# Kernel tuning notes

Hardware: AMD Instinct MI355X
Metric: run time of the kernel (lower is better)

Reference implementation:

```python
import jax, jax.numpy as jnp
import numpy as np


def setup_inputs() -> dict:
    key = jax.random.key(0)
    k1, k2, k3 = jax.random.split(key, 3)
    B, T, I, H = 32, 2048, 512, 512
    x = jax.random.normal(k1, (B, T, I), dtype=jnp.float32)
    W_x = jax.random.normal(k2, (3, I, H), dtype=jnp.float32) / np.sqrt(I)
    W_h = jax.random.normal(k3, (3, H, H), dtype=jnp.float32) / np.sqrt(H)
    bias = jnp.zeros((3, H), dtype=jnp.float32)
    return {"x": x, "W_x": W_x, "W_h": W_h, "bias": bias}


def reference(x, W_x, W_h, bias):
    # x: [B, T, I]; W_x: [3, I, H]; W_h: [3, H, H]; bias: [3, H]
    B, T, I = x.shape
    H = W_h.shape[-1]
    # Precompute input-side contributions for all gates/timesteps (batched GEMM):
    # gx: [T, 3, B, H] = x @ W_x[g] + bias[g]
    gx = jnp.einsum('bti,gih->tgbh', x, W_x) + bias[:, None, :]

    W_hz, W_hr, W_hh = W_h[0], W_h[1], W_h[2]

    def step(h_prev, gx_t):
        # gx_t: [3, B, H]
        z = jax.nn.sigmoid(gx_t[0] + h_prev @ W_hz)          # update gate
        r = jax.nn.sigmoid(gx_t[1] + h_prev @ W_hr)          # reset gate
        h_tilde = jnp.tanh(gx_t[2] + (r * h_prev) @ W_hh)    # candidate
        h_t = (1.0 - z) * h_prev + z * h_tilde
        return h_t, h_t

    h0 = jnp.zeros((B, H), dtype=x.dtype)
    h_last, outs = jax.lax.scan(step, h0, gx)  # outs: [T, B, H]
    output = jnp.transpose(outs, (1, 0, 2))    # [B, T, H]
    return output, h_last
```

## Files before the change

kernel.cpp:

```cpp
#include <hip/hip_runtime.h>
#include <stdint.h>
#include <stddef.h>


#define AGENT __HIP_MEMORY_SCOPE_AGENT

typedef _Float16 h2v __attribute__((ext_vector_type(2)));
typedef _Float16 half8 __attribute__((ext_vector_type(8)));
typedef float f32x4 __attribute__((ext_vector_type(4)));

__device__ __forceinline__ uint32_t pk2u(float a, float b) {
  h2v r; r[0] = (_Float16)a; r[1] = (_Float16)b;
  return __builtin_bit_cast(uint32_t, r);
}
__device__ __forceinline__ h2v bc2(uint32_t u) { return __builtin_bit_cast(h2v, u); }
__device__ __forceinline__ float dot2f(h2v a, h2v b, float c) {
#if __has_builtin(__builtin_amdgcn_fdot2)
  return __builtin_amdgcn_fdot2(a, b, c, false);
#else
  return fmaf((float)a[1], (float)b[1], fmaf((float)a[0], (float)b[0], c));
#endif
}
__device__ __forceinline__ float sigmoidf_(float x) { return 1.0f / (1.0f + __expf(-x)); }
__device__ __forceinline__ float tanhf_(float x) { return 1.0f - 2.0f / (1.0f + __expf(2.0f * x)); }
__device__ __forceinline__ uint64_t ald64(const uint64_t* p) {
  return __hip_atomic_load(p, __ATOMIC_RELAXED, AGENT);
}
__device__ __forceinline__ void ast64(uint64_t* p, uint64_t v) {
  __hip_atomic_store(p, v, __ATOMIC_RELAXED, AGENT);
}

__global__ __launch_bounds__(256) void gemm_gx(const float* __restrict__ x,
                                               const float* __restrict__ Wx,
                                               const float* __restrict__ bias,
                                               _Float16* gzr,
                                               _Float16* gh,
                                               int nTN) {
  __shared__ alignas(16) _Float16 Alds[128 * 68];
  __shared__ alignas(16) _Float16 Blds[128 * 68];
  const int tid = threadIdx.x;
  const int bid = blockIdx.x;
  const int tm = bid / nTN, tn = bid % nTN;
  const int m0 = tm << 7, n0 = tn << 7;
  const int lane = tid & 63;
  const int wv = tid >> 6, wm = wv >> 1, wn = wv & 1;
  const int l15 = lane & 15, lhi = lane >> 4;
  f32x4 acc[4][4] = {};

  for (int k0 = 0; k0 < 512; k0 += 64) {
#pragma unroll
    for (int r = 0; r < 8; ++r) {
      int m = r * 16 + (tid >> 4);
      int k = (tid & 15) * 4;
      float4 v = *(const float4*)&x[(size_t)(m0 + m) * 512 + k0 + k];
      union { _Float16 h[4]; uint2 u; } cv;
      cv.h[0] = (_Float16)v.x; cv.h[1] = (_Float16)v.y;
      cv.h[2] = (_Float16)v.z; cv.h[3] = (_Float16)v.w;
      *(uint2*)&Alds[m * 68 + k] = cv.u;
    }
#pragma unroll
    for (int u = 0; u < 8; ++u) {
      int n = tid & 127;
      int k = (tid >> 7) * 32 + u * 4;
      int ng = n0 + n;
      const float* wp = Wx + ((size_t)(ng >> 9) << 18) + (size_t)(k0 + k) * 512 + (ng & 511);
      union { _Float16 h[4]; uint2 u2; } cv;
      cv.h[0] = (_Float16)wp[0];    cv.h[1] = (_Float16)wp[512];
      cv.h[2] = (_Float16)wp[1024]; cv.h[3] = (_Float16)wp[1536];
      *(uint2*)&Blds[n * 68 + k] = cv.u2;
    }
    __syncthreads();
#pragma unroll
    for (int kk = 0; kk < 2; ++kk) {
      int q = kk * 4 + lhi;
      half8 af[4], bf[4];
#pragma unroll
      for (int fm = 0; fm < 4; ++fm) {
        const _Float16* pa = &Alds[(wm * 64 + fm * 16 + l15) * 68 + q * 8];
        union { uint2 u[2]; half8 h; } cv;
        cv.u[0] = *(const uint2*)pa; cv.u[1] = *(const uint2*)(pa + 4);
        af[fm] = cv.h;
      }
#pragma unroll
      for (int fn = 0; fn < 4; ++fn) {
        const _Float16* pb = &Blds[(wn * 64 + fn * 16 + l15) * 68 + q * 8];
        union { uint2 u[2]; half8 h; } cv;
        cv.u[0] = *(const uint2*)pb; cv.u[1] = *(const uint2*)(pb + 4);
        bf[fn] = cv.h;
      }
#pragma unroll
      for (int fm = 0; fm < 4; ++fm)
#pragma unroll
        for (int fn = 0; fn < 4; ++fn)
          acc[fm][fn] = __builtin_amdgcn_mfma_f32_16x16x32_f16(af[fm], bf[fn], acc[fm][fn], 0, 0, 0);
    }
    __syncthreads();
  }
#pragma unroll
  for (int fn = 0; fn < 4; ++fn) {
    int col = n0 + wn * 64 + fn * 16 + l15;
    float bv = bias[col];
#pragma unroll
    for (int fm = 0; fm < 4; ++fm) {
#pragma unroll
      for (int q2 = 0; q2 < 4; ++q2) {
        int row = m0 + wm * 64 + fm * 16 + lhi * 4 + q2;
        _Float16 val = (_Float16)(acc[fm][fn][q2] + bv);
        if (n0 < 1024) gzr[(size_t)row * 1024 + col] = val;
        else           gh[(size_t)row * 512 + (col - 1024)] = val;
      }
    }
  }
}

template <bool GH>
__global__ __launch_bounds__(512) void gru_scan(
    const float* __restrict__ x,
    const float* __restrict__ Wx,
    const float* __restrict__ Wh,
    const float* __restrict__ bias,
    const _Float16* gzr,
    const _Float16* gh,
    float* out,
    uint64_t* __restrict__ Pbuf,
    uint64_t* __restrict__ zbuf) {
  __shared__ alignas(16) float zrp[2][8][64];
  __shared__ alignas(16) _Float16 wzr[2 * 64 * 516];
  __shared__ alignas(16) _Float16 h16[512];
  __shared__ alignas(16) _Float16 rh16[64];
  __shared__ alignas(16) _Float16 x16s[64];

  const int T = threadIdx.x;
  const int bid = blockIdx.x;
  const int xcd = bid & 7, ii = bid >> 3;
  const int batch = xcd * 4 + (ii >> 3);
  const int slice = ii & 7;
  const int wv = T >> 6;
  const int ln = T & 63;
  const int n = T;

  {
    const int cc = T & 63, kb = T >> 6;
#pragma unroll 4
    for (int g = 0; g < 2; ++g) {
      const float* W = Wh + (size_t)g * 262144 + slice * 64 + cc;
      for (int i = 0; i < 64; ++i) {
        int k = kb + 8 * i;
        wzr[(g * 64 + cc) * 516 + k] = (_Float16)W[(size_t)k * 512];
      }
    }
  }
  uint32_t wh2[32], wx2[GH ? 1 : 32];
  {
    const float* Whh = Wh + 524288;
#pragma unroll
    for (int j = 0; j < 32; ++j) {
      int kk = slice * 64 + 2 * j;
      wh2[j] = pk2u(Whh[(size_t)kk * 512 + n], Whh[(size_t)(kk + 1) * 512 + n]);
    }
    if (!GH) {
      const float* Wxh = Wx + 524288;
#pragma unroll
      for (int j = 0; j < 32; ++j) {
        int kk = slice * 64 + 2 * j;
        wx2[j] = pk2u(Wxh[(size_t)kk * 512 + n], Wxh[(size_t)(kk + 1) * 512 + n]);
      }
    }
  }
  const float bh = bias[1024 + n];

  float hreg = 0.0f;
  h16[T] = (_Float16)0.0f;

  const size_t rowbase = (size_t)batch * 2048;
  float gz_p = 0.f, gr_p = 0.f, gz_cur = 0.f, gr_cur = 0.f, x_p = 0.f;
  float gh_p = 0.f, gh_cur = 0.f;
  if (T < 64)       gz_p = (float)gzr[rowbase * 1024 + slice * 64 + T];
  else if (T < 128) gr_p = (float)gzr[rowbase * 1024 + 512 + slice * 64 + (T - 64)];
  if (GH) gh_p = (float)gh[rowbase * 512 + n];
  else if (T < 64) x_p = x[rowbase * 512 + slice * 64 + T];

  uint64_t* Pmine = Pbuf + ((size_t)batch * 8 + slice) * 512 + n;
  const uint64_t* Pread = Pbuf + ((size_t)batch * 8) * 512 + n;
  uint64_t* zmine = zbuf + (size_t)batch * 512 + slice * 64 + ln;
  const uint64_t* zread = zbuf + (size_t)batch * 512 + n;

  for (int t = 0; t < 2048; ++t) {
    if (t > 0) {
      const size_t po = ((t - 1) & 1) ? 131072 : 0;
      const size_t zo = ((t - 1) & 1) ? 16384 : 0;
      const uint32_t want = (uint32_t)t;
      uint64_t v[8];
#pragma unroll
      for (int g = 0; g < 8; ++g) v[g] = ald64(Pread + po + (size_t)g * 512);
      uint64_t zv = ald64(zread + zo);
      for (;;) {
        bool ok = true;
        if ((uint32_t)(zv >> 32) != want) { zv = ald64(zread + zo); ok = false; }
#pragma unroll
        for (int g = 0; g < 8; ++g)
          if ((uint32_t)(v[g] >> 32) != want) { v[g] = ald64(Pread + po + (size_t)g * 512); ok = false; }
        if (ok) break;
        __builtin_amdgcn_s_sleep(1);
      }
      float hsum = 0.f;
#pragma unroll
      for (int g = 0; g < 8; ++g) hsum += __uint_as_float((uint32_t)v[g]);
      float zf = __uint_as_float((uint32_t)zv);
      float htil = tanhf_(GH ? (gh_cur + hsum) : (bh + hsum));
      float hn = fmaf(zf, htil - hreg, hreg);
      if (slice == 0) out[(rowbase + (t - 1)) * 512 + n] = hn;
      hreg = hn;
      h16[T] = (_Float16)hn;
    }
    gz_cur = gz_p; gr_cur = gr_p;
    if (GH) gh_cur = gh_p;
    else if (T < 64) x16s[T] = (_Float16)x_p;
    __syncthreads();
    if (t < 2047) {
      size_t r1 = rowbase + t + 1;
      if (T < 64)       gz_p = (float)gzr[r1 * 1024 + slice * 64 + T];
      else if (T < 128) gr_p = (float)gzr[r1 * 1024 + 512 + slice * 64 + (T - 64)];
      if (GH) gh_p = (float)gh[r1 * 512 + n];
      else if (T < 64) x_p = x[r1 * 512 + slice * 64 + T];
    }

    float za = 0.f, ra = 0.f;
    {
      const _Float16* wzp = &wzr[(0 * 64 + ln) * 516 + 64 * wv];
      const _Float16* wrp = &wzr[(1 * 64 + ln) * 516 + 64 * wv];
      const _Float16* hp = &h16[64 * wv];
#pragma unroll
      for (int j = 0; j < 16; ++j) {
        uint2 wzu = *(const uint2*)(wzp + 4 * j);
        uint2 wru = *(const uint2*)(wrp + 4 * j);
        uint2 hu = *(const uint2*)(hp + 4 * j);
        za = dot2f(bc2(hu.x), bc2(wzu.x), za);
        za = dot2f(bc2(hu.y), bc2(wzu.y), za);
        ra = dot2f(bc2(hu.x), bc2(wru.x), ra);
        ra = dot2f(bc2(hu.y), bc2(wru.y), ra);
      }
    }
    zrp[0][wv][ln] = za;
    zrp[1][wv][ln] = ra;
    __syncthreads();
    const size_t po = (t & 1) ? 131072 : 0;
    const size_t zo = (t & 1) ? 16384 : 0;
    const uint64_t tagw = ((uint64_t)(uint32_t)(t + 1)) << 32;
    if (T < 128) {
      const int g = T >> 6, c = T & 63;
      float sum = 0.f;
#pragma unroll
      for (int s2 = 0; s2 < 8; ++s2) sum += zrp[g][s2][c];
      if (g == 0) {
        float z = sigmoidf_(sum + gz_cur);
        ast64(zmine + zo, tagw | (uint32_t)__float_as_uint(z));
      } else {
        float r = sigmoidf_(sum + gr_cur);
        rh16[c] = (_Float16)(r * (float)h16[slice * 64 + c]);
      }
    }
    __syncthreads();

    float pa = 0.f;
#pragma unroll
    for (int j = 0; j < 16; ++j) {
      uint2 ru = *(const uint2*)&rh16[4 * j];
      pa = dot2f(bc2(ru.x), bc2(wh2[2 * j]), pa);
      pa = dot2f(bc2(ru.y), bc2(wh2[2 * j + 1]), pa);
    }
    if (!GH) {
#pragma unroll
      for (int j = 0; j < 16; ++j) {
        uint2 xu = *(const uint2*)&x16s[4 * j];
        pa = dot2f(bc2(xu.x), bc2(wx2[2 * j]), pa);
        pa = dot2f(bc2(xu.y), bc2(wx2[2 * j + 1]), pa);
      }
    }
    ast64(Pmine + po, tagw | (uint32_t)__float_as_uint(pa));
    if (!GH) __syncthreads();
  }

  {
    const uint32_t want = 2048u;
    uint64_t v[8];
#pragma unroll
    for (int g = 0; g < 8; ++g) v[g] = ald64(Pread + 131072 + (size_t)g * 512);
    uint64_t zv = ald64(zread + 16384);
    for (;;) {
      bool ok = true;
      if ((uint32_t)(zv >> 32) != want) { zv = ald64(zread + 16384); ok = false; }
#pragma unroll
      for (int g = 0; g < 8; ++g)
        if ((uint32_t)(v[g] >> 32) != want) { v[g] = ald64(Pread + 131072 + (size_t)g * 512); ok = false; }
      if (ok) break;
      __builtin_amdgcn_s_sleep(1);
    }
    float hsum = 0.f;
#pragma unroll
    for (int g = 0; g < 8; ++g) hsum += __uint_as_float((uint32_t)v[g]);
    float zf = __uint_as_float((uint32_t)zv);
    float htil = tanhf_(GH ? (gh_cur + hsum) : (bh + hsum));
    float hn = fmaf(zf, htil - hreg, hreg);
    if (slice == 0) {
      out[(rowbase + 2047) * 512 + n] = hn;
      out[(size_t)32 * 2048 * 512 + (size_t)batch * 512 + n] = hn;
    }
  }
}

extern "C" void kernel_launch(void* const* d_in, const int* in_sizes, int n_in,
                              void* d_out, int out_size, void* d_ws, size_t ws_size,
                              hipStream_t stream) {
  (void)in_sizes; (void)n_in; (void)out_size;
  const float* x    = (const float*)d_in[0];
  const float* Wx   = (const float*)d_in[1];
  const float* Wh   = (const float*)d_in[2];
  const float* bias = (const float*)d_in[3];
  float* out = (float*)d_out;
  char* ws = (char*)d_ws;

  uint64_t* Pbuf = (uint64_t*)ws;
  uint64_t* zbuf = (uint64_t*)(ws + 2097152);
  _Float16* gh   = (_Float16*)(ws + 2621440);

  hipMemsetAsync(ws, 0, 2621440, stream);
  const bool gh_mode = ws_size >= (size_t)2621440 + 67108864ull;
  if (gh_mode) {
    gemm_gx<<<512 * 12, 256, 0, stream>>>(x, Wx, bias, (_Float16*)d_out, gh, 12);
    gru_scan<true><<<256, 512, 0, stream>>>(x, Wx, Wh, bias, (const _Float16*)d_out,
                                            gh, out, Pbuf, zbuf);
  } else {
    gemm_gx<<<512 * 8, 256, 0, stream>>>(x, Wx, bias, (_Float16*)d_out, gh, 8);
    gru_scan<false><<<256, 512, 0, stream>>>(x, Wx, Wh, bias, (const _Float16*)d_out,
                                             gh, out, Pbuf, zbuf);
  }
}
```

Measured before the change: 7.110 ms.

## Split hidden dim over 16 blocks, interleave two batches per block

The persistent GRU scan kernel is restructured so each of 256 blocks owns a 32-column slice of the hidden state for two batches (16 slices per batch) instead of a 64-column slice for one batch. The two batches are processed in an interleaved way, so the cross-block wait for one batch's partial sums overlaps with compute for the other. The candidate partial sums are exchanged as fp16 values tagged with a 16-bit step number packed into 32-bit words, which halves exchange traffic. In exchange each step now reduces 16 partials instead of 8, adds more synchronisation points and lowers the precision of the exchanged partials.

```diff
diff --git a/kernel.cpp b/kernel.cpp
--- a/kernel.cpp
+++ b/kernel.cpp
@@ -23,11 +23,21 @@
 }
 __device__ __forceinline__ float sigmoidf_(float x) { return 1.0f / (1.0f + __expf(-x)); }
 __device__ __forceinline__ float tanhf_(float x) { return 1.0f - 2.0f / (1.0f + __expf(2.0f * x)); }
+
+__device__ __forceinline__ uint32_t ald32(const uint32_t* p) {
+  return __hip_atomic_load(p, __ATOMIC_RELAXED, AGENT);
+}
+__device__ __forceinline__ void ast32(uint32_t* p, uint32_t v) {
+  __hip_atomic_store(p, v, __ATOMIC_RELAXED, AGENT);
+}
 __device__ __forceinline__ uint64_t ald64(const uint64_t* p) {
   return __hip_atomic_load(p, __ATOMIC_RELAXED, AGENT);
 }
 __device__ __forceinline__ void ast64(uint64_t* p, uint64_t v) {
   __hip_atomic_store(p, v, __ATOMIC_RELAXED, AGENT);
+}
+__device__ __forceinline__ float f16b2f(uint32_t w) {
+  return (float)__builtin_bit_cast(_Float16, (unsigned short)(w & 0xffffu));
 }
 
 __global__ __launch_bounds__(256) void gemm_gx(const float* __restrict__ x,
@@ -113,19 +123,293 @@
   }
 }
 
-template <bool GH>
-__global__ __launch_bounds__(512) void gru_scan(
-    const float* __restrict__ x,
-    const float* __restrict__ Wx,
+__device__ __forceinline__ bool tagsok(const uint32_t pv[16], uint64_t zv, uint32_t want) {
+  bool ok = ((uint32_t)(zv >> 32) == want);
+#pragma unroll
+  for (int q = 0; q < 16; ++q) ok &= ((pv[q] >> 16) == want);
+  return ok;
+}
+
+__global__ __launch_bounds__(512) void gru_scan2(
+    const _Float16* gzr,
+    const _Float16* ghg,
     const float* __restrict__ Wh,
-    const float* __restrict__ bias,
-    const _Float16* gzr,
-    const _Float16* gh,
     float* out,
-    uint64_t* __restrict__ Pbuf,
+    uint32_t* __restrict__ Pbuf,
     uint64_t* __restrict__ zbuf) {
+  __shared__ alignas(16) _Float16 wzK[2 * 64 * 32 * 8];
+  __shared__ alignas(16) _Float16 hA[512], hB[512];
+  __shared__ alignas(16) _Float16 rhA[32], rhB[32];
+  __shared__ alignas(16) float zrp[2][16][32];
+
+  const int T = threadIdx.x;
+  const int bid = blockIdx.x;
+  const int s = bid >> 4;
+  const int p = bid & 15;
+  const int c0 = s * 32;
+  const int bA = p, bB = p + 16;
+  const int j = T & 31, sub = T >> 5;
+
+  for (int g = 0; g < 2; ++g) {
+    const float* W = Wh + (size_t)g * 262144;
+    for (int kc = sub; kc < 64; kc += 16) {
+#pragma unroll
+      for (int e = 0; e < 8; ++e) {
+        int k = kc * 8 + e;
+        wzK[((g * 64 + kc) * 32 + j) * 8 + e] = (_Float16)W[(size_t)k * 512 + c0 + j];
+      }
+    }
+  }
+  uint32_t wh2[16];
+  {
+    const float* Whh = Wh + 524288;
+#pragma unroll
+    for (int i = 0; i < 16; ++i) {
+      int kk = c0 + 2 * i;
+      wh2[i] = pk2u(Whh[(size_t)kk * 512 + T], Whh[(size_t)(kk + 1) * 512 + T]);
+    }
+  }
+  hA[T] = (_Float16)0.0f;
+  hB[T] = (_Float16)0.0f;
+  float hregA = 0.f, hregB = 0.f;
+
+  const size_t rbA = (size_t)bA * 2048, rbB = (size_t)bB * 2048;
+  float gzA_p = 0.f, grA_p = 0.f, gzB_p = 0.f, grB_p = 0.f;
+  float gzA_c = 0.f, grA_c = 0.f, gzB_c = 0.f, grB_c = 0.f;
+  float ghA_p, ghB_p, ghA_c = 0.f, ghB_c = 0.f;
+  if (T < 32) {
+    gzA_p = (float)gzr[rbA * 1024 + c0 + T];
+    gzB_p = (float)gzr[rbB * 1024 + c0 + T];
+  } else if (T < 64) {
+    grA_p = (float)gzr[rbA * 1024 + 512 + c0 + (T - 32)];
+    grB_p = (float)gzr[rbB * 1024 + 512 + c0 + (T - 32)];
+  }
+  ghA_p = (float)ghg[rbA * 512 + T];
+  ghB_p = (float)ghg[rbB * 512 + T];
+
+  uint32_t* PmA = Pbuf + ((size_t)bA * 512 + T) * 16 + s;
+  uint32_t* PmB = Pbuf + ((size_t)bB * 512 + T) * 16 + s;
+  const uint32_t* PrA = Pbuf + ((size_t)bA * 512 + T) * 16;
+  const uint32_t* PrB = Pbuf + ((size_t)bB * 512 + T) * 16;
+  uint64_t* zmA = zbuf + (size_t)bA * 512 + c0 + (T & 31);
+  uint64_t* zmB = zbuf + (size_t)bB * 512 + c0 + (T & 31);
+  const uint64_t* zrdA = zbuf + (size_t)bA * 512 + T;
+  const uint64_t* zrdB = zbuf + (size_t)bB * 512 + T;
+
+  uint32_t pvA[16], pvB[16];
+  uint64_t zvA = 0, zvB = 0;
+#pragma unroll
+  for (int q = 0; q < 16; ++q) { pvA[q] = 0; pvB[q] = 0; }
+
+  for (int t = 0; t < 2048; ++t) {
+    const size_t poC = ((t - 1) & 1) ? 262144 : 0;
+    const size_t zoC = ((t - 1) & 1) ? 16384 : 0;
+    const size_t poN = (t & 1) ? 262144 : 0;
+    const size_t zoN = (t & 1) ? 16384 : 0;
+    const uint32_t want = (uint32_t)t;
+    const uint32_t tagN = (uint32_t)(t + 1);
+
+    if (t > 0) {
+      while (!tagsok(pvA, zvA, want)) {
+        __builtin_amdgcn_s_sleep(1);
+        zvA = ald64(zrdA + zoC);
+#pragma unroll
+        for (int q = 0; q < 16; ++q)
+          if ((pvA[q] >> 16) != want) pvA[q] = ald32(PrA + poC + q);
+      }
+      float hsum = 0.f;
+#pragma unroll
+      for (int q = 0; q < 16; ++q) hsum += f16b2f(pvA[q]);
+      float zf = __uint_as_float((uint32_t)zvA);
+      float htil = tanhf_(ghA_c + hsum);
+      float hn = fmaf(zf, htil - hregA, hregA);
+      if (sub == s) out[(rbA + (t - 1)) * 512 + T] = hn;
+      hregA = hn;
+      hA[T] = (_Float16)hn;
+    }
+    gzA_c = gzA_p; grA_c = grA_p; ghA_c = ghA_p;
+    __syncthreads();
+    if (t < 2047) {
+      size_t r1 = rbA + t + 1;
+      if (T < 32)      gzA_p = (float)gzr[r1 * 1024 + c0 + T];
+      else if (T < 64) grA_p = (float)gzr[r1 * 1024 + 512 + c0 + (T - 32)];
+      ghA_p = (float)ghg[r1 * 512 + T];
+    }
+    {
+      float za = 0.f, ra = 0.f;
+#pragma unroll
+      for (int cc = 0; cc < 4; ++cc) {
+        int kc = sub * 4 + cc;
+        uint4 hu = *(const uint4*)&hA[kc * 8];
+        uint4 wz = *(const uint4*)&wzK[(kc * 32 + j) * 8];
+        uint4 wr = *(const uint4*)&wzK[((64 + kc) * 32 + j) * 8];
+        za = dot2f(bc2(hu.x), bc2(wz.x), za); za = dot2f(bc2(hu.y), bc2(wz.y), za);
+        za = dot2f(bc2(hu.z), bc2(wz.z), za); za = dot2f(bc2(hu.w), bc2(wz.w), za);
+        ra = dot2f(bc2(hu.x), bc2(wr.x), ra); ra = dot2f(bc2(hu.y), bc2(wr.y), ra);
+        ra = dot2f(bc2(hu.z), bc2(wr.z), ra); ra = dot2f(bc2(hu.w), bc2(wr.w), ra);
+      }
+      zrp[0][sub][j] = za;
+      zrp[1][sub][j] = ra;
+    }
+    if (t > 0) {
+      zvB = ald64(zrdB + zoC);
+#pragma unroll
+      for (int q = 0; q < 16; ++q) pvB[q] = ald32(PrB + poC + q);
+    }
+    __syncthreads();
+    if (T < 64) {
+      const int g = T >> 5, jj = T & 31;
+      float sum = 0.f;
+#pragma unroll
+      for (int q = 0; q < 16; ++q) sum += zrp[g][q][jj];
+      if (g == 0) {
+        float z = sigmoidf_(sum + gzA_c);
+        ast64(zmA + zoN, ((uint64_t)tagN << 32) | (uint32_t)__float_as_uint(z));
+      } else {
+        float r = sigmoidf_(sum + grA_c);
+        rhA[jj] = (_Float16)(r * (float)hA[c0 + jj]);
+      }
+    }
+    __syncthreads();
+    {
+      float pa = 0.f;
+#pragma unroll
+      for (int i = 0; i < 8; ++i) {
+        uint2 ru = *(const uint2*)&rhA[4 * i];
+        pa = dot2f(bc2(ru.x), bc2(wh2[2 * i]), pa);
+        pa = dot2f(bc2(ru.y), bc2(wh2[2 * i + 1]), pa);
+      }
+      unsigned short pb = __builtin_bit_cast(unsigned short, (_Float16)pa);
+      ast32(PmA + poN, (tagN << 16) | (uint32_t)pb);
+    }
+
+    if (t > 0) {
+      while (!tagsok(pvB, zvB, want)) {
+        __builtin_amdgcn_s_sleep(1);
+        zvB = ald64(zrdB + zoC);
+#pragma unroll
+        for (int q = 0; q < 16; ++q)
+          if ((pvB[q] >> 16) != want) pvB[q] = ald32(PrB + poC + q);
+      }
+      float hsum = 0.f;
+#pragma unroll
+      for (int q = 0; q < 16; ++q) hsum += f16b2f(pvB[q]);
+      float zf = __uint_as_float((uint32_t)zvB);
+      float htil = tanhf_(ghB_c + hsum);
+      float hn = fmaf(zf, htil - hregB, hregB);
+      if (sub == s) out[(rbB + (t - 1)) * 512 + T] = hn;
+      hregB = hn;
+      hB[T] = (_Float16)hn;
+    }
+    gzB_c = gzB_p; grB_c = grB_p; ghB_c = ghB_p;
+    __syncthreads();
+    if (t < 2047) {
+      size_t r1 = rbB + t + 1;
+      if (T < 32)      gzB_p = (float)gzr[r1 * 1024 + c0 + T];
+      else if (T < 64) grB_p = (float)gzr[r1 * 1024 + 512 + c0 + (T - 32)];
+      ghB_p = (float)ghg[r1 * 512 + T];
+    }
+    {
+      float za = 0.f, ra = 0.f;
+#pragma unroll
+      for (int cc = 0; cc < 4; ++cc) {
+        int kc = sub * 4 + cc;
+        uint4 hu = *(const uint4*)&hB[kc * 8];
+        uint4 wz = *(const uint4*)&wzK[(kc * 32 + j) * 8];
+        uint4 wr = *(const uint4*)&wzK[((64 + kc) * 32 + j) * 8];
+        za = dot2f(bc2(hu.x), bc2(wz.x), za); za = dot2f(bc2(hu.y), bc2(wz.y), za);
+        za = dot2f(bc2(hu.z), bc2(wz.z), za); za = dot2f(bc2(hu.w), bc2(wz.w), za);
+        ra = dot2f(bc2(hu.x), bc2(wr.x), ra); ra = dot2f(bc2(hu.y), bc2(wr.y), ra);
+        ra = dot2f(bc2(hu.z), bc2(wr.z), ra); ra = dot2f(bc2(hu.w), bc2(wr.w), ra);
+      }
+      zrp[0][sub][j] = za;
+      zrp[1][sub][j] = ra;
+    }
+    {
+      zvA = ald64(zrdA + zoN);
+#pragma unroll
+      for (int q = 0; q < 16; ++q) pvA[q] = ald32(PrA + poN + q);
+    }
+    __syncthreads();
+    if (T < 64) {
+      const int g = T >> 5, jj = T & 31;
+      float sum = 0.f;
+#pragma unroll
+      for (int q = 0; q < 16; ++q) sum += zrp[g][q][jj];
+      if (g == 0) {
+        float z = sigmoidf_(sum + gzB_c);
+        ast64(zmB + zoN, ((uint64_t)tagN << 32) | (uint32_t)__float_as_uint(z));
+      } else {
+        float r = sigmoidf_(sum + grB_c);
+        rhB[jj] = (_Float16)(r * (float)hB[c0 + jj]);
+      }
+    }
+    __syncthreads();
+    {
+      float pa = 0.f;
+#pragma unroll
+      for (int i = 0; i < 8; ++i) {
+        uint2 ru = *(const uint2*)&rhB[4 * i];
+        pa = dot2f(bc2(ru.x), bc2(wh2[2 * i]), pa);
+        pa = dot2f(bc2(ru.y), bc2(wh2[2 * i + 1]), pa);
+      }
+      unsigned short pb = __builtin_bit_cast(unsigned short, (_Float16)pa);
+      ast32(PmB + poN, (tagN << 16) | (uint32_t)pb);
+    }
+  }
+
+  {
+    const uint32_t want = 2048u;
+    while (!tagsok(pvA, zvA, want)) {
+      __builtin_amdgcn_s_sleep(1);
+      zvA = ald64(zrdA + 16384);
+#pragma unroll
+      for (int q = 0; q < 16; ++q)
+        if ((pvA[q] >> 16) != want) pvA[q] = ald32(PrA + 262144 + q);
+    }
+    float hsum = 0.f;
+#pragma unroll
+    for (int q = 0; q < 16; ++q) hsum += f16b2f(pvA[q]);
+    float zf = __uint_as_float((uint32_t)zvA);
+    float htil = tanhf_(ghA_c + hsum);
+    float hn = fmaf(zf, htil - hregA, hregA);
+    if (sub == s) {
+      out[(rbA + 2047) * 512 + T] = hn;
+      out[(size_t)32 * 2048 * 512 + (size_t)bA * 512 + T] = hn;
+    }
+  }
+  {
+    const uint32_t want = 2048u;
+    zvB = ald64(zrdB + 16384);
+#pragma unroll
+    for (int q = 0; q < 16; ++q) pvB[q] = ald32(PrB + 262144 + q);
+    while (!tagsok(pvB, zvB, want)) {
+      __builtin_amdgcn_s_sleep(1);
+      zvB = ald64(zrdB + 16384);
+#pragma unroll
+      for (int q = 0; q < 16; ++q)
+        if ((pvB[q] >> 16) != want) pvB[q] = ald32(PrB + 262144 + q);
+    }
+    float hsum = 0.f;
+#pragma unroll
+    for (int q = 0; q < 16; ++q) hsum += f16b2f(pvB[q]);
+    float zf = __uint_as_float((uint32_t)zvB);
+    float htil = tanhf_(ghB_c + hsum);
+    float hn = fmaf(zf, htil - hregB, hregB);
+    if (sub == s) {
+      out[(rbB + 2047) * 512 + T] = hn;
+      out[(size_t)32 * 2048 * 512 + (size_t)bB * 512 + T] = hn;
+    }
+  }
+}
+
+__global__ __launch_bounds__(512) void gru_scan_fb(
+    const float* __restrict__ x, const float* __restrict__ Wx,
+    const float* __restrict__ Wh, const float* __restrict__ bias,
+    const _Float16* gzr, float* out,
+    uint64_t* __restrict__ Pbuf, uint64_t* __restrict__ zbuf) {
   __shared__ alignas(16) float zrp[2][8][64];
-  __shared__ alignas(16) _Float16 wzr[2 * 64 * 516];
+  __shared__ alignas(16) _Float16 wzrL[2 * 64 * 516];
   __shared__ alignas(16) _Float16 h16[512];
   __shared__ alignas(16) _Float16 rh16[64];
   __shared__ alignas(16) _Float16 x16s[64];
@@ -135,10 +419,7 @@
   const int xcd = bid & 7, ii = bid >> 3;
   const int batch = xcd * 4 + (ii >> 3);
   const int slice = ii & 7;
-  const int wv = T >> 6;
-  const int ln = T & 63;
-  const int n = T;
-
+  const int wv = T >> 6, ln = T & 63, n = T;
   {
     const int cc = T & 63, kb = T >> 6;
 #pragma unroll 4
@@ -146,39 +427,29 @@
       const float* W = Wh + (size_t)g * 262144 + slice * 64 + cc;
       for (int i = 0; i < 64; ++i) {
         int k = kb + 8 * i;
-        wzr[(g * 64 + cc) * 516 + k] = (_Float16)W[(size_t)k * 512];
-      }
-    }
-  }
-  uint32_t wh2[32], wx2[GH ? 1 : 32];
+        wzrL[(g * 64 + cc) * 516 + k] = (_Float16)W[(size_t)k * 512];
+      }
+    }
+  }
+  uint32_t wh2[32], wx2[32];
   {
     const float* Whh = Wh + 524288;
-#pragma unroll
-    for (int j = 0; j < 32; ++j) {
-      int kk = slice * 64 + 2 * j;
-      wh2[j] = pk2u(Whh[(size_t)kk * 512 + n], Whh[(size_t)(kk + 1) * 512 + n]);
-    }
-    if (!GH) {
-      const float* Wxh = Wx + 524288;
-#pragma unroll
-      for (int j = 0; j < 32; ++j) {
-        int kk = slice * 64 + 2 * j;
-        wx2[j] = pk2u(Wxh[(size_t)kk * 512 + n], Wxh[(size_t)(kk + 1) * 512 + n]);
-      }
+    const float* Wxh = Wx + 524288;
+#pragma unroll
+    for (int jj = 0; jj < 32; ++jj) {
+      int kk = slice * 64 + 2 * jj;
+      wh2[jj] = pk2u(Whh[(size_t)kk * 512 + n], Whh[(size_t)(kk + 1) * 512 + n]);
+      wx2[jj] = pk2u(Wxh[(size_t)kk * 512 + n], Wxh[(size_t)(kk + 1) * 512 + n]);
     }
   }
   const float bh = bias[1024 + n];
-
   float hreg = 0.0f;
   h16[T] = (_Float16)0.0f;
-
   const size_t rowbase = (size_t)batch * 2048;
   float gz_p = 0.f, gr_p = 0.f, gz_cur = 0.f, gr_cur = 0.f, x_p = 0.f;
-  float gh_p = 0.f, gh_cur = 0.f;
   if (T < 64)       gz_p = (float)gzr[rowbase * 1024 + slice * 64 + T];
   else if (T < 128) gr_p = (float)gzr[rowbase * 1024 + 512 + slice * 64 + (T - 64)];
-  if (GH) gh_p = (float)gh[rowbase * 512 + n];
-  else if (T < 64) x_p = x[rowbase * 512 + slice * 64 + T];
+  if (T < 64) x_p = x[rowbase * 512 + slice * 64 + T];
 
   uint64_t* Pmine = Pbuf + ((size_t)batch * 8 + slice) * 512 + n;
   const uint64_t* Pread = Pbuf + ((size_t)batch * 8) * 512 + n;
@@ -207,34 +478,31 @@
 #pragma unroll
       for (int g = 0; g < 8; ++g) hsum += __uint_as_float((uint32_t)v[g]);
       float zf = __uint_as_float((uint32_t)zv);
-      float htil = tanhf_(GH ? (gh_cur + hsum) : (bh + hsum));
+      float htil = tanhf_(bh + hsum);
       float hn = fmaf(zf, htil - hreg, hreg);
       if (slice == 0) out[(rowbase + (t - 1)) * 512 + n] = hn;
       hreg = hn;
       h16[T] = (_Float16)hn;
     }
     gz_cur = gz_p; gr_cur = gr_p;
-    if (GH) gh_cur = gh_p;
-    else if (T < 64) x16s[T] = (_Float16)x_p;
+    if (T < 64) x16s[T] = (_Float16)x_p;
     __syncthreads();
     if (t < 2047) {
       size_t r1 = rowbase + t + 1;
       if (T < 64)       gz_p = (float)gzr[r1 * 1024 + slice * 64 + T];
       else if (T < 128) gr_p = (float)gzr[r1 * 1024 + 512 + slice * 64 + (T - 64)];
-      if (GH) gh_p = (float)gh[r1 * 512 + n];
-      else if (T < 64) x_p = x[r1 * 512 + slice * 64 + T];
-    }
-
+      if (T < 64) x_p = x[r1 * 512 + slice * 64 + T];
+    }
     float za = 0.f, ra = 0.f;
     {
-      const _Float16* wzp = &wzr[(0 * 64 + ln) * 516 + 64 * wv];
-      const _Float16* wrp = &wzr[(1 * 64 + ln) * 516 + 64 * wv];
+      const _Float16* wzp = &wzrL[ln * 516 + 64 * wv];
+      const _Float16* wrp = &wzrL[(64 + ln) * 516 + 64 * wv];
       const _Float16* hp = &h16[64 * wv];
 #pragma unroll
-      for (int j = 0; j < 16; ++j) {
-        uint2 wzu = *(const uint2*)(wzp + 4 * j);
-        uint2 wru = *(const uint2*)(wrp + 4 * j);
-        uint2 hu = *(const uint2*)(hp + 4 * j);
+      for (int jj = 0; jj < 16; ++jj) {
+        uint2 wzu = *(const uint2*)(wzp + 4 * jj);
+        uint2 wru = *(const uint2*)(wrp + 4 * jj);
+        uint2 hu = *(const uint2*)(hp + 4 * jj);
         za = dot2f(bc2(hu.x), bc2(wzu.x), za);
         za = dot2f(bc2(hu.y), bc2(wzu.y), za);
         ra = dot2f(bc2(hu.x), bc2(wru.x), ra);
@@ -248,39 +516,35 @@
     const size_t zo = (t & 1) ? 16384 : 0;
     const uint64_t tagw = ((uint64_t)(uint32_t)(t + 1)) << 32;
     if (T < 128) {
-      const int g = T >> 6, c = T & 63;
+      const int g = T >> 6, cc = T & 63;
       float sum = 0.f;
 #pragma unroll
-      for (int s2 = 0; s2 < 8; ++s2) sum += zrp[g][s2][c];
+      for (int s2 = 0; s2 < 8; ++s2) sum += zrp[g][s2][cc];
       if (g == 0) {
         float z = sigmoidf_(sum + gz_cur);
         ast64(zmine + zo, tagw | (uint32_t)__float_as_uint(z));
       } else {
         float r = sigmoidf_(sum + gr_cur);
-        rh16[c] = (_Float16)(r * (float)h16[slice * 64 + c]);
-      }
-    }
-    __syncthreads();
-
+        rh16[cc] = (_Float16)(r * (float)h16[slice * 64 + cc]);
+      }
+    }
+    __syncthreads();
     float pa = 0.f;
 #pragma unroll
-    for (int j = 0; j < 16; ++j) {
-      uint2 ru = *(const uint2*)&rh16[4 * j];
-      pa = dot2f(bc2(ru.x), bc2(wh2[2 * j]), pa);
-      pa = dot2f(bc2(ru.y), bc2(wh2[2 * j + 1]), pa);
-    }
-    if (!GH) {
-#pragma unroll
-      for (int j = 0; j < 16; ++j) {
-        uint2 xu = *(const uint2*)&x16s[4 * j];
-        pa = dot2f(bc2(xu.x), bc2(wx2[2 * j]), pa);
-        pa = dot2f(bc2(xu.y), bc2(wx2[2 * j + 1]), pa);
-      }
+    for (int jj = 0; jj < 16; ++jj) {
+      uint2 ru = *(const uint2*)&rh16[4 * jj];
+      pa = dot2f(bc2(ru.x), bc2(wh2[2 * jj]), pa);
+      pa = dot2f(bc2(ru.y), bc2(wh2[2 * jj + 1]), pa);
+    }
+#pragma unroll
+    for (int jj = 0; jj < 16; ++jj) {
+      uint2 xu = *(const uint2*)&x16s[4 * jj];
+      pa = dot2f(bc2(xu.x), bc2(wx2[2 * jj]), pa);
+      pa = dot2f(bc2(xu.y), bc2(wx2[2 * jj + 1]), pa);
     }
     ast64(Pmine + po, tagw | (uint32_t)__float_as_uint(pa));
-    if (!GH) __syncthreads();
-  }
-
+    __syncthreads();
+  }
   {
     const uint32_t want = 2048u;
     uint64_t v[8];
@@ -300,7 +564,7 @@
 #pragma unroll
     for (int g = 0; g < 8; ++g) hsum += __uint_as_float((uint32_t)v[g]);
     float zf = __uint_as_float((uint32_t)zv);
-    float htil = tanhf_(GH ? (gh_cur + hsum) : (bh + hsum));
+    float htil = tanhf_(bh + hsum);
     float hn = fmaf(zf, htil - hreg, hreg);
     if (slice == 0) {
       out[(rowbase + 2047) * 512 + n] = hn;
@@ -320,19 +584,21 @@
   float* out = (float*)d_out;
   char* ws = (char*)d_ws;
 
-  uint64_t* Pbuf = (uint64_t*)ws;
-  uint64_t* zbuf = (uint64_t*)(ws + 2097152);
-  _Float16* gh   = (_Float16*)(ws + 2621440);
+  uint32_t* Pbuf2 = (uint32_t*)ws;
+  uint64_t* zbuf2 = (uint64_t*)(ws + 2097152);
+  uint64_t* PbufF = (uint64_t*)ws;
+  uint64_t* zbufF = (uint64_t*)(ws + 2097152);
+  _Float16* gh    = (_Float16*)(ws + 2621440);
 
   hipMemsetAsync(ws, 0, 2621440, stream);
   const bool gh_mode = ws_size >= (size_t)2621440 + 67108864ull;
   if (gh_mode) {
     gemm_gx<<<512 * 12, 256, 0, stream>>>(x, Wx, bias, (_Float16*)d_out, gh, 12);
-    gru_scan<true><<<256, 512, 0, stream>>>(x, Wx, Wh, bias, (const _Float16*)d_out,
-                                            gh, out, Pbuf, zbuf);
+    gru_scan2<<<256, 512, 0, stream>>>((const _Float16*)d_out, gh, Wh, out,
+                                       Pbuf2, zbuf2);
   } else {
     gemm_gx<<<512 * 8, 256, 0, stream>>>(x, Wx, bias, (_Float16*)d_out, gh, 8);
-    gru_scan<false><<<256, 512, 0, stream>>>(x, Wx, Wh, bias, (const _Float16*)d_out,
-                                             gh, out, Pbuf, zbuf);
-  }
-}
+    gru_scan_fb<<<256, 512, 0, stream>>>(x, Wx, Wh, bias, (const _Float16*)d_out,
+                                         out, PbufF, zbufF);
+  }
+}
```

Result: slower. 23.25 ms (+227.0%).

## Restructure GRU scan with packed fp16 partial tags, shuffle reduction and early polling

Applied to the files above, without the earlier changes.

Replaces the gh-mode scan kernel with a new version. It packs each partial sum as fp16 plus a 16-bit tag in one 32-bit word, which halves cross-block exchange traffic. The z/r gate matvec is redone with 8 threads per column and a warp-shuffle reduction, dropping one shared-memory reduction stage and one barrier per step. The poll loads for the next step are issued right after the stores, so their latency overlaps the loop tail. It also remaps blocks to slice-major order. The cost is lower precision on the partials (fp16 sums) and a narrower tag range, which still covers 2048 steps.

```diff
diff --git a/kernel.cpp b/kernel.cpp
--- a/kernel.cpp
+++ b/kernel.cpp
@@ -23,11 +23,21 @@
 }
 __device__ __forceinline__ float sigmoidf_(float x) { return 1.0f / (1.0f + __expf(-x)); }
 __device__ __forceinline__ float tanhf_(float x) { return 1.0f - 2.0f / (1.0f + __expf(2.0f * x)); }
+
+__device__ __forceinline__ uint32_t ald32(const uint32_t* p) {
+  return __hip_atomic_load(p, __ATOMIC_RELAXED, AGENT);
+}
+__device__ __forceinline__ void ast32(uint32_t* p, uint32_t v) {
+  __hip_atomic_store(p, v, __ATOMIC_RELAXED, AGENT);
+}
 __device__ __forceinline__ uint64_t ald64(const uint64_t* p) {
   return __hip_atomic_load(p, __ATOMIC_RELAXED, AGENT);
 }
 __device__ __forceinline__ void ast64(uint64_t* p, uint64_t v) {
   __hip_atomic_store(p, v, __ATOMIC_RELAXED, AGENT);
+}
+__device__ __forceinline__ float f16b2f(uint32_t w) {
+  return (float)__builtin_bit_cast(_Float16, (unsigned short)(w & 0xffffu));
 }
 
 __global__ __launch_bounds__(256) void gemm_gx(const float* __restrict__ x,
@@ -113,19 +123,183 @@
   }
 }
 
-template <bool GH>
-__global__ __launch_bounds__(512) void gru_scan(
-    const float* __restrict__ x,
-    const float* __restrict__ Wx,
+__device__ __forceinline__ bool tagsok8(const uint32_t pv[8], uint64_t zv, uint32_t want) {
+  bool ok = ((uint32_t)(zv >> 32) == want);
+#pragma unroll
+  for (int q = 0; q < 8; ++q) ok &= ((pv[q] >> 16) == want);
+  return ok;
+}
+
+__global__ __launch_bounds__(512) void gru_scan3(
+    const _Float16* gzr,
+    const _Float16* ghg,
     const float* __restrict__ Wh,
-    const float* __restrict__ bias,
-    const _Float16* gzr,
-    const _Float16* gh,
     float* out,
-    uint64_t* __restrict__ Pbuf,
+    uint32_t* __restrict__ Pbuf,
     uint64_t* __restrict__ zbuf) {
+  __shared__ alignas(16) _Float16 wzK[2 * 8 * 64 * 8 * 8];
+  __shared__ alignas(16) _Float16 hA[512];
+  __shared__ alignas(16) _Float16 rh[64];
+
+  const int T = threadIdx.x;
+  const int bid = blockIdx.x;
+  const int s = bid >> 5;
+  const int b = bid & 31;
+  const int c = T >> 3, sub = T & 7;
+  const int gcol = s * 64 + c;
+
+  for (int g = 0; g < 2; ++g) {
+    const float* W = Wh + (size_t)g * 262144;
+    for (int idx = T; idx < 4096; idx += 512) {
+      int cc = idx >> 9;
+      int col = (idx >> 3) & 63;
+      int sb = idx & 7;
+      int kbase = (cc * 8 + sb) * 8;
+      _Float16* dst = &wzK[(((g * 8 + cc) * 64 + col) * 8 + sb) * 8];
+#pragma unroll
+      for (int e = 0; e < 8; ++e)
+        dst[e] = (_Float16)W[(size_t)(kbase + e) * 512 + s * 64 + col];
+    }
+  }
+  uint32_t wh2[32];
+  {
+    const float* Whh = Wh + 524288;
+#pragma unroll
+    for (int i = 0; i < 32; ++i) {
+      int kk = s * 64 + 2 * i;
+      wh2[i] = pk2u(Whh[(size_t)kk * 512 + T], Whh[(size_t)(kk + 1) * 512 + T]);
+    }
+  }
+  hA[T] = (_Float16)0.0f;
+  float hreg = 0.f;
+
+  const size_t rb = (size_t)b * 2048;
+  float gh_p, gh_c = 0.f, gz_p = 0.f, gr_p = 0.f, gz_c = 0.f, gr_c = 0.f;
+  gh_p = (float)ghg[rb * 512 + T];
+  if (sub == 0) {
+    gz_p = (float)gzr[rb * 1024 + gcol];
+    gr_p = (float)gzr[rb * 1024 + 512 + gcol];
+  }
+
+  uint32_t* Pm = Pbuf + ((size_t)b * 8 + s) * 512 + T;
+  const uint32_t* Pr = Pbuf + (size_t)b * 4096 + T;
+  uint64_t* zm = zbuf + (size_t)b * 512 + gcol;
+  const uint64_t* zrd = zbuf + (size_t)b * 512 + T;
+
+  uint32_t pv[8];
+  uint64_t zv = 0;
+#pragma unroll
+  for (int q = 0; q < 8; ++q) pv[q] = 0;
+
+  for (int t = 0; t < 2048; ++t) {
+    const size_t poC = ((t - 1) & 1) ? 131072 : 0;
+    const size_t zoC = ((t - 1) & 1) ? 16384 : 0;
+    const size_t poN = (t & 1) ? 131072 : 0;
+    const size_t zoN = (t & 1) ? 16384 : 0;
+    const uint32_t want = (uint32_t)t;
+    const uint32_t tagN = (uint32_t)(t + 1);
+
+    if (t > 0) {
+      while (!tagsok8(pv, zv, want)) {
+        __builtin_amdgcn_s_sleep(2);
+        if ((uint32_t)(zv >> 32) != want) zv = ald64(zrd + zoC);
+#pragma unroll
+        for (int q = 0; q < 8; ++q)
+          if ((pv[q] >> 16) != want) pv[q] = ald32(Pr + poC + (size_t)q * 512);
+      }
+      float hsum = 0.f;
+#pragma unroll
+      for (int q = 0; q < 8; ++q) hsum += f16b2f(pv[q]);
+      float zf = __uint_as_float((uint32_t)zv);
+      float htil = tanhf_(gh_c + hsum);
+      float hn = fmaf(zf, htil - hreg, hreg);
+      if (s == 0) out[(rb + (t - 1)) * 512 + T] = hn;
+      hreg = hn;
+      hA[T] = (_Float16)hn;
+    }
+    gh_c = gh_p;
+    gz_c = gz_p;
+    gr_c = gr_p;
+    __syncthreads();
+    if (t < 2047) {
+      size_t r1 = rb + t + 1;
+      gh_p = (float)ghg[r1 * 512 + T];
+      if (sub == 0) {
+        gz_p = (float)gzr[r1 * 1024 + gcol];
+        gr_p = (float)gzr[r1 * 1024 + 512 + gcol];
+      }
+    }
+
+    float za = 0.f, ra = 0.f;
+#pragma unroll
+    for (int cc = 0; cc < 8; ++cc) {
+      uint4 hu = *(const uint4*)&hA[(cc * 8 + sub) * 8];
+      uint4 wz = *(const uint4*)&wzK[(((cc)*64 + c) * 8 + sub) * 8];
+      uint4 wr = *(const uint4*)&wzK[(((8 + cc) * 64 + c) * 8 + sub) * 8];
+      za = dot2f(bc2(hu.x), bc2(wz.x), za); za = dot2f(bc2(hu.y), bc2(wz.y), za);
+      za = dot2f(bc2(hu.z), bc2(wz.z), za); za = dot2f(bc2(hu.w), bc2(wz.w), za);
+      ra = dot2f(bc2(hu.x), bc2(wr.x), ra); ra = dot2f(bc2(hu.y), bc2(wr.y), ra);
+      ra = dot2f(bc2(hu.z), bc2(wr.z), ra); ra = dot2f(bc2(hu.w), bc2(wr.w), ra);
+    }
+#pragma unroll
+    for (int d = 1; d < 8; d <<= 1) {
+      za += __shfl_xor(za, d);
+      ra += __shfl_xor(ra, d);
+    }
+    if (sub == 0) {
+      float z = sigmoidf_(za + gz_c);
+      float r = sigmoidf_(ra + gr_c);
+      rh[c] = (_Float16)(r * (float)hA[gcol]);
+      ast64(zm + zoN, ((uint64_t)tagN << 32) | (uint32_t)__float_as_uint(z));
+    }
+    __syncthreads();
+
+    {
+      float pa = 0.f;
+#pragma unroll
+      for (int i = 0; i < 16; ++i) {
+        uint2 ru = *(const uint2*)&rh[4 * i];
+        pa = dot2f(bc2(ru.x), bc2(wh2[2 * i]), pa);
+        pa = dot2f(bc2(ru.y), bc2(wh2[2 * i + 1]), pa);
+      }
+      unsigned short pb = __builtin_bit_cast(unsigned short, (_Float16)pa);
+      ast32(Pm + poN, (tagN << 16) | (uint32_t)pb);
+    }
+    zv = ald64(zrd + zoN);
+#pragma unroll
+    for (int q = 0; q < 8; ++q) pv[q] = ald32(Pr + poN + (size_t)q * 512);
+    __builtin_amdgcn_sched_barrier(0);
+  }
+
+  {
+    const uint32_t want = 2048u;
+    while (!tagsok8(pv, zv, want)) {
+      __builtin_amdgcn_s_sleep(2);
+      if ((uint32_t)(zv >> 32) != want) zv = ald64(zrd + 16384);
+#pragma unroll
+      for (int q = 0; q < 8; ++q)
+        if ((pv[q] >> 16) != want) pv[q] = ald32(Pr + 131072 + (size_t)q * 512);
+    }
+    float hsum = 0.f;
+#pragma unroll
+    for (int q = 0; q < 8; ++q) hsum += f16b2f(pv[q]);
+    float zf = __uint_as_float((uint32_t)zv);
+    float htil = tanhf_(gh_c + hsum);
+    float hn = fmaf(zf, htil - hreg, hreg);
+    if (s == 0) {
+      out[(rb + 2047) * 512 + T] = hn;
+      out[(size_t)32 * 2048 * 512 + (size_t)b * 512 + T] = hn;
+    }
+  }
+}
+
+__global__ __launch_bounds__(512) void gru_scan_fb(
+    const float* __restrict__ x, const float* __restrict__ Wx,
+    const float* __restrict__ Wh, const float* __restrict__ bias,
+    const _Float16* gzr, float* out,
+    uint64_t* __restrict__ Pbuf, uint64_t* __restrict__ zbuf) {
   __shared__ alignas(16) float zrp[2][8][64];
-  __shared__ alignas(16) _Float16 wzr[2 * 64 * 516];
+  __shared__ alignas(16) _Float16 wzrL[2 * 64 * 516];
   __shared__ alignas(16) _Float16 h16[512];
   __shared__ alignas(16) _Float16 rh16[64];
   __shared__ alignas(16) _Float16 x16s[64];
@@ -135,10 +309,7 @@
   const int xcd = bid & 7, ii = bid >> 3;
   const int batch = xcd * 4 + (ii >> 3);
   const int slice = ii & 7;
-  const int wv = T >> 6;
-  const int ln = T & 63;
-  const int n = T;
-
+  const int wv = T >> 6, ln = T & 63, n = T;
   {
     const int cc = T & 63, kb = T >> 6;
 #pragma unroll 4
@@ -146,39 +317,29 @@
       const float* W = Wh + (size_t)g * 262144 + slice * 64 + cc;
       for (int i = 0; i < 64; ++i) {
         int k = kb + 8 * i;
-        wzr[(g * 64 + cc) * 516 + k] = (_Float16)W[(size_t)k * 512];
-      }
-    }
-  }
-  uint32_t wh2[32], wx2[GH ? 1 : 32];
+        wzrL[(g * 64 + cc) * 516 + k] = (_Float16)W[(size_t)k * 512];
+      }
+    }
+  }
+  uint32_t wh2[32], wx2[32];
   {
     const float* Whh = Wh + 524288;
-#pragma unroll
-    for (int j = 0; j < 32; ++j) {
-      int kk = slice * 64 + 2 * j;
-      wh2[j] = pk2u(Whh[(size_t)kk * 512 + n], Whh[(size_t)(kk + 1) * 512 + n]);
-    }
-    if (!GH) {
-      const float* Wxh = Wx + 524288;
-#pragma unroll
-      for (int j = 0; j < 32; ++j) {
-        int kk = slice * 64 + 2 * j;
-        wx2[j] = pk2u(Wxh[(size_t)kk * 512 + n], Wxh[(size_t)(kk + 1) * 512 + n]);
-      }
+    const float* Wxh = Wx + 524288;
+#pragma unroll
+    for (int jj = 0; jj < 32; ++jj) {
+      int kk = slice * 64 + 2 * jj;
+      wh2[jj] = pk2u(Whh[(size_t)kk * 512 + n], Whh[(size_t)(kk + 1) * 512 + n]);
+      wx2[jj] = pk2u(Wxh[(size_t)kk * 512 + n], Wxh[(size_t)(kk + 1) * 512 + n]);
     }
   }
   const float bh = bias[1024 + n];
-
   float hreg = 0.0f;
   h16[T] = (_Float16)0.0f;
-
   const size_t rowbase = (size_t)batch * 2048;
   float gz_p = 0.f, gr_p = 0.f, gz_cur = 0.f, gr_cur = 0.f, x_p = 0.f;
-  float gh_p = 0.f, gh_cur = 0.f;
   if (T < 64)       gz_p = (float)gzr[rowbase * 1024 + slice * 64 + T];
   else if (T < 128) gr_p = (float)gzr[rowbase * 1024 + 512 + slice * 64 + (T - 64)];
-  if (GH) gh_p = (float)gh[rowbase * 512 + n];
-  else if (T < 64) x_p = x[rowbase * 512 + slice * 64 + T];
+  if (T < 64) x_p = x[rowbase * 512 + slice * 64 + T];
 
   uint64_t* Pmine = Pbuf + ((size_t)batch * 8 + slice) * 512 + n;
   const uint64_t* Pread = Pbuf + ((size_t)batch * 8) * 512 + n;
@@ -193,10 +354,10 @@
       uint64_t v[8];
 #pragma unroll
       for (int g = 0; g < 8; ++g) v[g] = ald64(Pread + po + (size_t)g * 512);
-      uint64_t zv = ald64(zread + zo);
+      uint64_t zvv = ald64(zread + zo);
       for (;;) {
         bool ok = true;
-        if ((uint32_t)(zv >> 32) != want) { zv = ald64(zread + zo); ok = false; }
+        if ((uint32_t)(zvv >> 32) != want) { zvv = ald64(zread + zo); ok = false; }
 #pragma unroll
         for (int g = 0; g < 8; ++g)
           if ((uint32_t)(v[g] >> 32) != want) { v[g] = ald64(Pread + po + (size_t)g * 512); ok = false; }
@@ -206,35 +367,32 @@
       float hsum = 0.f;
 #pragma unroll
       for (int g = 0; g < 8; ++g) hsum += __uint_as_float((uint32_t)v[g]);
-      float zf = __uint_as_float((uint32_t)zv);
-      float htil = tanhf_(GH ? (gh_cur + hsum) : (bh + hsum));
+      float zf = __uint_as_float((uint32_t)zvv);
+      float htil = tanhf_(bh + hsum);
       float hn = fmaf(zf, htil - hreg, hreg);
       if (slice == 0) out[(rowbase + (t - 1)) * 512 + n] = hn;
       hreg = hn;
       h16[T] = (_Float16)hn;
     }
     gz_cur = gz_p; gr_cur = gr_p;
-    if (GH) gh_cur = gh_p;
-    else if (T < 64) x16s[T] = (_Float16)x_p;
+    if (T < 64) x16s[T] = (_Float16)x_p;
     __syncthreads();
     if (t < 2047) {
       size_t r1 = rowbase + t + 1;
       if (T < 64)       gz_p = (float)gzr[r1 * 1024 + slice * 64 + T];
       else if (T < 128) gr_p = (float)gzr[r1 * 1024 + 512 + slice * 64 + (T - 64)];
-      if (GH) gh_p = (float)gh[r1 * 512 + n];
-      else if (T < 64) x_p = x[r1 * 512 + slice * 64 + T];
-    }
-
+      if (T < 64) x_p = x[r1 * 512 + slice * 64 + T];
+    }
     float za = 0.f, ra = 0.f;
     {
-      const _Float16* wzp = &wzr[(0 * 64 + ln) * 516 + 64 * wv];
-      const _Float16* wrp = &wzr[(1 * 64 + ln) * 516 + 64 * wv];
+      const _Float16* wzp = &wzrL[ln * 516 + 64 * wv];
+      const _Float16* wrp = &wzrL[(64 + ln) * 516 + 64 * wv];
       const _Float16* hp = &h16[64 * wv];
 #pragma unroll
-      for (int j = 0; j < 16; ++j) {
-        uint2 wzu = *(const uint2*)(wzp + 4 * j);
-        uint2 wru = *(const uint2*)(wrp + 4 * j);
-        uint2 hu = *(const uint2*)(hp + 4 * j);
+      for (int jj = 0; jj < 16; ++jj) {
+        uint2 wzu = *(const uint2*)(wzp + 4 * jj);
+        uint2 wru = *(const uint2*)(wrp + 4 * jj);
+        uint2 hu = *(const uint2*)(hp + 4 * jj);
         za = dot2f(bc2(hu.x), bc2(wzu.x), za);
         za = dot2f(bc2(hu.y), bc2(wzu.y), za);
         ra = dot2f(bc2(hu.x), bc2(wru.x), ra);
@@ -248,48 +406,44 @@
     const size_t zo = (t & 1) ? 16384 : 0;
     const uint64_t tagw = ((uint64_t)(uint32_t)(t + 1)) << 32;
     if (T < 128) {
-      const int g = T >> 6, c = T & 63;
+      const int g = T >> 6, cc = T & 63;
       float sum = 0.f;
 #pragma unroll
-      for (int s2 = 0; s2 < 8; ++s2) sum += zrp[g][s2][c];
+      for (int s2 = 0; s2 < 8; ++s2) sum += zrp[g][s2][cc];
       if (g == 0) {
         float z = sigmoidf_(sum + gz_cur);
         ast64(zmine + zo, tagw | (uint32_t)__float_as_uint(z));
       } else {
         float r = sigmoidf_(sum + gr_cur);
-        rh16[c] = (_Float16)(r * (float)h16[slice * 64 + c]);
-      }
-    }
-    __syncthreads();
-
+        rh16[cc] = (_Float16)(r * (float)h16[slice * 64 + cc]);
+      }
+    }
+    __syncthreads();
     float pa = 0.f;
 #pragma unroll
-    for (int j = 0; j < 16; ++j) {
-      uint2 ru = *(const uint2*)&rh16[4 * j];
-      pa = dot2f(bc2(ru.x), bc2(wh2[2 * j]), pa);
-      pa = dot2f(bc2(ru.y), bc2(wh2[2 * j + 1]), pa);
-    }
-    if (!GH) {
-#pragma unroll
-      for (int j = 0; j < 16; ++j) {
-        uint2 xu = *(const uint2*)&x16s[4 * j];
-        pa = dot2f(bc2(xu.x), bc2(wx2[2 * j]), pa);
-        pa = dot2f(bc2(xu.y), bc2(wx2[2 * j + 1]), pa);
-      }
+    for (int jj = 0; jj < 16; ++jj) {
+      uint2 ru = *(const uint2*)&rh16[4 * jj];
+      pa = dot2f(bc2(ru.x), bc2(wh2[2 * jj]), pa);
+      pa = dot2f(bc2(ru.y), bc2(wh2[2 * jj + 1]), pa);
+    }
+#pragma unroll
+    for (int jj = 0; jj < 16; ++jj) {
+      uint2 xu = *(const uint2*)&x16s[4 * jj];
+      pa = dot2f(bc2(xu.x), bc2(wx2[2 * jj]), pa);
+      pa = dot2f(bc2(xu.y), bc2(wx2[2 * jj + 1]), pa);
     }
     ast64(Pmine + po, tagw | (uint32_t)__float_as_uint(pa));
-    if (!GH) __syncthreads();
-  }
-
+    __syncthreads();
+  }
   {
     const uint32_t want = 2048u;
     uint64_t v[8];
 #pragma unroll
     for (int g = 0; g < 8; ++g) v[g] = ald64(Pread + 131072 + (size_t)g * 512);
-    uint64_t zv = ald64(zread + 16384);
+    uint64_t zvv = ald64(zread + 16384);
     for (;;) {
       bool ok = true;
-      if ((uint32_t)(zv >> 32) != want) { zv = ald64(zread + 16384); ok = false; }
+      if ((uint32_t)(zvv >> 32) != want) { zvv = ald64(zread + 16384); ok = false; }
 #pragma unroll
       for (int g = 0; g < 8; ++g)
         if ((uint32_t)(v[g] >> 32) != want) { v[g] = ald64(Pread + 131072 + (size_t)g * 512); ok = false; }
@@ -299,8 +453,8 @@
     float hsum = 0.f;
 #pragma unroll
     for (int g = 0; g < 8; ++g) hsum += __uint_as_float((uint32_t)v[g]);
-    float zf = __uint_as_float((uint32_t)zv);
-    float htil = tanhf_(GH ? (gh_cur + hsum) : (bh + hsum));
+    float zf = __uint_as_float((uint32_t)zvv);
+    float htil = tanhf_(bh + hsum);
     float hn = fmaf(zf, htil - hreg, hreg);
     if (slice == 0) {
       out[(rowbase + 2047) * 512 + n] = hn;
@@ -320,19 +474,21 @@
   float* out = (float*)d_out;
   char* ws = (char*)d_ws;
 
-  uint64_t* Pbuf = (uint64_t*)ws;
-  uint64_t* zbuf = (uint64_t*)(ws + 2097152);
-  _Float16* gh   = (_Float16*)(ws + 2621440);
+  uint32_t* Pbuf3 = (uint32_t*)ws;
+  uint64_t* zbuf3 = (uint64_t*)(ws + 1048576);
+  uint64_t* PbufF = (uint64_t*)ws;
+  uint64_t* zbufF = (uint64_t*)(ws + 2097152);
+  _Float16* gh    = (_Float16*)(ws + 2621440);
 
   hipMemsetAsync(ws, 0, 2621440, stream);
   const bool gh_mode = ws_size >= (size_t)2621440 + 67108864ull;
   if (gh_mode) {
     gemm_gx<<<512 * 12, 256, 0, stream>>>(x, Wx, bias, (_Float16*)d_out, gh, 12);
-    gru_scan<true><<<256, 512, 0, stream>>>(x, Wx, Wh, bias, (const _Float16*)d_out,
-                                            gh, out, Pbuf, zbuf);
+    gru_scan3<<<256, 512, 0, stream>>>((const _Float16*)d_out, gh, Wh, out,
+                                       Pbuf3, zbuf3);
   } else {
     gemm_gx<<<512 * 8, 256, 0, stream>>>(x, Wx, bias, (_Float16*)d_out, gh, 8);
-    gru_scan<false><<<256, 512, 0, stream>>>(x, Wx, Wh, bias, (const _Float16*)d_out,
-                                             gh, out, Pbuf, zbuf);
-  }
-}
+    gru_scan_fb<<<256, 512, 0, stream>>>(x, Wx, Wh, bias, (const _Float16*)d_out,
+                                         out, PbufF, zbufF);
+  }
+}
```

Result: no change. 7.155 ms (median of 2 runs) (+0.6%).
